# Performance work log

Hardware: AMD Instinct MI355X
Metric: run time of the kernel (lower is better)

Reference implementation:

```python
import jax, jax.numpy as jnp
import numpy as np

N = 100000   # nodes
E = 1000000  # edges
F_IN = 128
H = 64
L = 6
C = 10
G = 64       # graphs in batch


def setup_inputs() -> dict:
    key = jax.random.key(0)
    ks = jax.random.split(key, 12)
    x = jax.random.normal(ks[0], (N, F_IN), dtype=jnp.float32)
    edge_index = jax.random.randint(ks[1], (2, E), 0, N, dtype=jnp.int64)
    batch = jnp.sort(jax.random.randint(ks[2], (N,), 0, G, dtype=jnp.int64))
    s = lambda fan: 1.0 / np.sqrt(fan)
    return {
        "x": x,
        "edge_index": edge_index,
        "batch": batch,
        "W0": jax.random.normal(ks[3], (F_IN, H), dtype=jnp.float32) * s(F_IN),
        "b0": jnp.zeros((H,), jnp.float32),
        "Wh": jax.random.normal(ks[4], (L - 1, H, H), dtype=jnp.float32) * s(H),
        "bh": jnp.zeros((L - 1, H), jnp.float32),
        "jkW": jax.random.normal(ks[5], (H * L, H), dtype=jnp.float32) * s(H * L),
        "jkb": jnp.zeros((H,), jnp.float32),
        "W1": jax.random.normal(ks[6], (H, H), dtype=jnp.float32) * s(H),
        "b1": jnp.zeros((H,), jnp.float32),
        "W2": jax.random.normal(ks[7], (H, C), dtype=jnp.float32) * s(H),
        "b2": jnp.zeros((C,), jnp.float32),
    }


def reference(x, edge_index, batch, W0, b0, Wh, bh, jkW, jkb, W1, b1, W2, b2):
    n = x.shape[0]
    # add self-loops (PyG GCNConv default)
    loops = jnp.arange(n, dtype=edge_index.dtype)
    src = jnp.concatenate([edge_index[0], loops])
    dst = jnp.concatenate([edge_index[1], loops])
    # symmetric degree normalization D^{-1/2} (A+I) D^{-1/2}
    deg = jax.ops.segment_sum(jnp.ones_like(dst, x.dtype), dst, num_segments=n)
    disq = jnp.where(deg > 0, deg ** -0.5, 0.0)
    norm = (disq[src] * disq[dst])[:, None]  # [E+N, 1]

    def gcn(h, W, b):
        hW = h @ W                              # [N, H] transform first
        msg = hW[src] * norm                    # gather + normalize
        agg = jax.ops.segment_sum(msg, dst, num_segments=n)  # scatter-add
        return agg + b

    h = jax.nn.relu(gcn(x, W0, b0))
    xs = [h]
    for i in range(L - 1):
        h = jax.nn.relu(gcn(h, Wh[i], bh[i]))
        xs.append(h)
    hcat = jnp.concatenate(xs, axis=-1)         # JK 'cat' -> [N, H*L]
    h = jax.nn.relu(hcat @ jkW + jkb)
    pooled = jax.ops.segment_sum(h, batch, num_segments=G)  # global_add_pool
    h = jax.nn.relu(pooled @ W1 + b1)
    return jax.nn.softmax(h @ W2 + b2, axis=-1)  # [G, C]
```

## Files before the change

kernel.cpp:

```cpp
#include <hip/hip_runtime.h>
#include <hip/hip_fp16.h>

#define NN 100000
#define NE 1000000
#define F_INF 128
#define HID 64
#define NLAY 6
#define NCLS 10
#define NGRAPH 64
#define PART_SZ 12500

__device__ __forceinline__ float4 h4f(ushort4 u) {
    __half2 lo = *reinterpret_cast<__half2*>(&u);
    __half2 hi = *reinterpret_cast<__half2*>(reinterpret_cast<unsigned short*>(&u) + 2);
    float2 a = __half22float2(lo);
    float2 b = __half22float2(hi);
    return make_float4(a.x, a.y, b.x, b.y);
}

__device__ __forceinline__ ushort4 f4h(float4 v) {
    __half2 lo = __floats2half2_rn(v.x, v.y);
    __half2 hi = __floats2half2_rn(v.z, v.w);
    ushort4 u;
    *reinterpret_cast<__half2*>(&u) = lo;
    *reinterpret_cast<__half2*>(reinterpret_cast<unsigned short*>(&u) + 2) = hi;
    return u;
}

__global__ void k_hist(const int* __restrict__ dst, int* __restrict__ counts, int e) {
    int i = blockIdx.x * 256 + threadIdx.x;
    if (i < e) atomicAdd(&counts[dst[i]], 1);
}

__global__ void k_blocksum(const int* __restrict__ counts, int* __restrict__ bsum, int n) {
    int i = blockIdx.x * 256 + threadIdx.x;
    int v = (i < n) ? counts[i] : 0;
    #pragma unroll
    for (int off = 32; off >= 1; off >>= 1) v += __shfl_down(v, off);
    __shared__ int ws[4];
    if ((threadIdx.x & 63) == 0) ws[threadIdx.x >> 6] = v;
    __syncthreads();
    if (threadIdx.x == 0) bsum[blockIdx.x] = ws[0] + ws[1] + ws[2] + ws[3];
}

__global__ void k_scanbsum(int* __restrict__ bsum, int nb) {
    __shared__ int sh[512];
    int t = threadIdx.x;
    int v = (t < nb) ? bsum[t] : 0;
    sh[t] = v; __syncthreads();
    for (int off = 1; off < 512; off <<= 1) {
        int x = (t >= off) ? sh[t - off] : 0;
        __syncthreads();
        sh[t] += x; __syncthreads();
    }
    if (t < nb) bsum[t] = sh[t] - v;
}

__global__ void k_scanwrite(const int* __restrict__ counts, const int* __restrict__ bsumx,
                            int* __restrict__ rowptr, int* __restrict__ wptr,
                            float* __restrict__ disq, int n, int e) {
    __shared__ int sh[256];
    int t = threadIdx.x;
    int i = blockIdx.x * 256 + t;
    int v = (i < n) ? counts[i] : 0;
    sh[t] = v; __syncthreads();
    for (int off = 1; off < 256; off <<= 1) {
        int x = (t >= off) ? sh[t - off] : 0;
        __syncthreads();
        sh[t] += x; __syncthreads();
    }
    int excl = sh[t] - v + bsumx[blockIdx.x];
    if (i < n) {
        rowptr[i] = excl;
        wptr[i]   = excl;
        disq[i]   = rsqrtf((float)(v + 1));
    }
    if (i == 0) rowptr[n] = e;
}

__global__ void k_scatter_part(const int* __restrict__ src, const int* __restrict__ dst,
                               int* __restrict__ wptr, int* __restrict__ csr, int e) {
    int part = blockIdx.x & 7;
    int i = (blockIdx.x >> 3) * 256 + threadIdx.x;
    if (i < e) {
        int d = dst[i];
        if (d / PART_SZ == part) {
            int pos = atomicAdd(&wptr[d], 1);
            csr[pos] = src[i];
        }
    }
}

__global__ __launch_bounds__(256) void k_gemm_dual(
    const float* __restrict__ A, int lda, int K,
    const float* __restrict__ W,
    const float* __restrict__ jkw,
    const float* __restrict__ disq,
    unsigned short* __restrict__ C16,
    float* __restrict__ jkacc,
    int jk_mode, int n)
{
    __shared__ float Ws[64 * 64];
    __shared__ float Ws2[64 * 64];
    __shared__ float As[64 * 68];
    const int tid  = threadIdx.x;
    const int col4 = (tid & 15) * 4;
    const int rowq = tid >> 4;
    const int base = blockIdx.x * 64;

    {
        #pragma unroll
        for (int i = 0; i < 4; i++) {
            float4 v = *(const float4*)(W + (size_t)(i * 256 + tid) * 4);
            *(float4*)(Ws + (size_t)(i * 256 + tid) * 4) = v;
        }
        if (jk_mode) {
            #pragma unroll
            for (int i = 0; i < 4; i++) {
                float4 v = *(const float4*)(jkw + (size_t)(i * 256 + tid) * 4);
                *(float4*)(Ws2 + (size_t)(i * 256 + tid) * 4) = v;
            }
        }
        #pragma unroll
        for (int rr = 0; rr < 4; rr++) {
            int row = base + rowq + rr * 16;
            float4 v = make_float4(0.f, 0.f, 0.f, 0.f);
            if (row < n) v = *(const float4*)(A + (size_t)row * lda + col4);
            *(float4*)(As + (size_t)(rowq + rr * 16) * 68 + col4) = v;
        }
    }
    __syncthreads();

    float4 acc[4], acc2[4];
    #pragma unroll
    for (int r = 0; r < 4; r++) {
        acc[r]  = make_float4(0.f, 0.f, 0.f, 0.f);
        acc2[r] = make_float4(0.f, 0.f, 0.f, 0.f);
    }

    for (int k0 = 0; k0 < K; k0 += 64) {
        const bool more = (k0 + 64) < K;
        float4 wreg[4], areg[4];
        if (more) {
            #pragma unroll
            for (int i = 0; i < 4; i++)
                wreg[i] = *(const float4*)(W + (size_t)(k0 + 64) * 64 + (i * 256 + tid) * 4);
            #pragma unroll
            for (int rr = 0; rr < 4; rr++) {
                int row = base + rowq + rr * 16;
                areg[rr] = make_float4(0.f, 0.f, 0.f, 0.f);
                if (row < n) areg[rr] = *(const float4*)(A + (size_t)row * lda + k0 + 64 + col4);
            }
        }
        if (jk_mode && k0 == 0) {
            #pragma unroll 4
            for (int k = 0; k < 64; k++) {
                float4 w  = *(const float4*)(Ws  + k * 64 + col4);
                float4 w2 = *(const float4*)(Ws2 + k * 64 + col4);
                float a0 = As[(rowq * 4 + 0) * 68 + k];
                float a1 = As[(rowq * 4 + 1) * 68 + k];
                float a2 = As[(rowq * 4 + 2) * 68 + k];
                float a3 = As[(rowq * 4 + 3) * 68 + k];
                acc[0].x = fmaf(a0, w.x, acc[0].x); acc[0].y = fmaf(a0, w.y, acc[0].y);
                acc[0].z = fmaf(a0, w.z, acc[0].z); acc[0].w = fmaf(a0, w.w, acc[0].w);
                acc[1].x = fmaf(a1, w.x, acc[1].x); acc[1].y = fmaf(a1, w.y, acc[1].y);
                acc[1].z = fmaf(a1, w.z, acc[1].z); acc[1].w = fmaf(a1, w.w, acc[1].w);
                acc[2].x = fmaf(a2, w.x, acc[2].x); acc[2].y = fmaf(a2, w.y, acc[2].y);
                acc[2].z = fmaf(a2, w.z, acc[2].z); acc[2].w = fmaf(a2, w.w, acc[2].w);
                acc[3].x = fmaf(a3, w.x, acc[3].x); acc[3].y = fmaf(a3, w.y, acc[3].y);
                acc[3].z = fmaf(a3, w.z, acc[3].z); acc[3].w = fmaf(a3, w.w, acc[3].w);
                acc2[0].x = fmaf(a0, w2.x, acc2[0].x); acc2[0].y = fmaf(a0, w2.y, acc2[0].y);
                acc2[0].z = fmaf(a0, w2.z, acc2[0].z); acc2[0].w = fmaf(a0, w2.w, acc2[0].w);
                acc2[1].x = fmaf(a1, w2.x, acc2[1].x); acc2[1].y = fmaf(a1, w2.y, acc2[1].y);
                acc2[1].z = fmaf(a1, w2.z, acc2[1].z); acc2[1].w = fmaf(a1, w2.w, acc2[1].w);
                acc2[2].x = fmaf(a2, w2.x, acc2[2].x); acc2[2].y = fmaf(a2, w2.y, acc2[2].y);
                acc2[2].z = fmaf(a2, w2.z, acc2[2].z); acc2[2].w = fmaf(a2, w2.w, acc2[2].w);
                acc2[3].x = fmaf(a3, w2.x, acc2[3].x); acc2[3].y = fmaf(a3, w2.y, acc2[3].y);
                acc2[3].z = fmaf(a3, w2.z, acc2[3].z); acc2[3].w = fmaf(a3, w2.w, acc2[3].w);
            }
        } else {
            #pragma unroll 8
            for (int k = 0; k < 64; k++) {
                float4 w = *(const float4*)(Ws + k * 64 + col4);
                float a0 = As[(rowq * 4 + 0) * 68 + k];
                float a1 = As[(rowq * 4 + 1) * 68 + k];
                float a2 = As[(rowq * 4 + 2) * 68 + k];
                float a3 = As[(rowq * 4 + 3) * 68 + k];
                acc[0].x = fmaf(a0, w.x, acc[0].x); acc[0].y = fmaf(a0, w.y, acc[0].y);
                acc[0].z = fmaf(a0, w.z, acc[0].z); acc[0].w = fmaf(a0, w.w, acc[0].w);
                acc[1].x = fmaf(a1, w.x, acc[1].x); acc[1].y = fmaf(a1, w.y, acc[1].y);
                acc[1].z = fmaf(a1, w.z, acc[1].z); acc[1].w = fmaf(a1, w.w, acc[1].w);
                acc[2].x = fmaf(a2, w.x, acc[2].x); acc[2].y = fmaf(a2, w.y, acc[2].y);
                acc[2].z = fmaf(a2, w.z, acc[2].z); acc[2].w = fmaf(a2, w.w, acc[2].w);
                acc[3].x = fmaf(a3, w.x, acc[3].x); acc[3].y = fmaf(a3, w.y, acc[3].y);
                acc[3].z = fmaf(a3, w.z, acc[3].z); acc[3].w = fmaf(a3, w.w, acc[3].w);
            }
        }
        __syncthreads();
        if (more) {
            #pragma unroll
            for (int i = 0; i < 4; i++)
                *(float4*)(Ws + (size_t)(i * 256 + tid) * 4) = wreg[i];
            #pragma unroll
            for (int rr = 0; rr < 4; rr++)
                *(float4*)(As + (size_t)(rowq + rr * 16) * 68 + col4) = areg[rr];
            __syncthreads();
        }
    }

    #pragma unroll
    for (int r = 0; r < 4; r++) {
        int row = base + rowq * 4 + r;
        if (row < n) {
            float s = disq[row];
            float4 o;
            o.x = acc[r].x * s; o.y = acc[r].y * s;
            o.z = acc[r].z * s; o.w = acc[r].w * s;
            ((ushort4*)C16)[(size_t)row * 16 + (tid & 15)] = f4h(o);
            if (jk_mode == 1) {
                *(float4*)(jkacc + (size_t)row * 64 + col4) = acc2[r];
            } else if (jk_mode == 2) {
                float4 p = *(const float4*)(jkacc + (size_t)row * 64 + col4);
                p.x += acc2[r].x; p.y += acc2[r].y;
                p.z += acc2[r].z; p.w += acc2[r].w;
                *(float4*)(jkacc + (size_t)row * 64 + col4) = p;
            }
        }
    }
}

__global__ __launch_bounds__(256) void k_gather(
    const int* __restrict__ rowptr, const int* __restrict__ csr,
    const unsigned short* __restrict__ hW16, const float* __restrict__ disq,
    const float* __restrict__ bias, float* __restrict__ hout, int n)
{
    const ushort4* hW4 = (const ushort4*)hW16;
    int wid  = (blockIdx.x * 256 + threadIdx.x) >> 6;
    if (wid >= n) return;
    int lane = threadIdx.x & 63;
    int fb = lane & 15;
    int es = lane >> 4;
    int j  = rowptr[wid];
    int r1 = rowptr[wid + 1];
    float4 v  = make_float4(0.f, 0.f, 0.f, 0.f);
    float4 v2 = make_float4(0.f, 0.f, 0.f, 0.f);
    if (es == 0) v = h4f(hW4[(size_t)wid * 16 + fb]);
    while (j < r1) {
        int cnt = min(r1 - j, 64);
        int idx = (lane < cnt) ? csr[j + lane] : 0;
        int jj = 0;
        for (; jj + 8 <= cnt; jj += 8) {
            int s0 = __shfl(idx, jj + es);
            int s1 = __shfl(idx, jj + 4 + es);
            float4 t0 = h4f(hW4[(size_t)s0 * 16 + fb]);
            float4 t1 = h4f(hW4[(size_t)s1 * 16 + fb]);
            v.x  += t0.x; v.y  += t0.y; v.z  += t0.z; v.w  += t0.w;
            v2.x += t1.x; v2.y += t1.y; v2.z += t1.z; v2.w += t1.w;
        }
        for (; jj < cnt; jj += 4) {
            int sidx = jj + es;
            int s = __shfl(idx, (sidx < cnt) ? sidx : 0);
            if (sidx < cnt) {
                float4 t = h4f(hW4[(size_t)s * 16 + fb]);
                v.x += t.x; v.y += t.y; v.z += t.z; v.w += t.w;
            }
        }
        j += cnt;
    }
    v.x += v2.x; v.y += v2.y; v.z += v2.z; v.w += v2.w;
    v.x += __shfl_xor(v.x, 16); v.y += __shfl_xor(v.y, 16);
    v.z += __shfl_xor(v.z, 16); v.w += __shfl_xor(v.w, 16);
    v.x += __shfl_xor(v.x, 32); v.y += __shfl_xor(v.y, 32);
    v.z += __shfl_xor(v.z, 32); v.w += __shfl_xor(v.w, 32);
    if (es == 0) {
        float s = disq[wid];
        float4 b = ((const float4*)bias)[fb];
        float4 o;
        o.x = fmaxf(fmaf(s, v.x, b.x), 0.f);
        o.y = fmaxf(fmaf(s, v.y, b.y), 0.f);
        o.z = fmaxf(fmaf(s, v.z, b.z), 0.f);
        o.w = fmaxf(fmaf(s, v.w, b.w), 0.f);
        ((float4*)hout)[(size_t)wid * 16 + fb] = o;
    }
}

__global__ __launch_bounds__(256) void k_jkfin_pool(
    const float* __restrict__ A,
    const float* __restrict__ W,
    const float* __restrict__ jkacc,
    const float* __restrict__ bias,
    const int* __restrict__ batch,
    float* __restrict__ pooled,
    int n)
{
    __shared__ float Ws[64 * 64];
    __shared__ float As[64 * 68];
    const int tid  = threadIdx.x;
    const int col4 = (tid & 15) * 4;
    const int rowq = tid >> 4;
    const int base = blockIdx.x * 64;

    #pragma unroll
    for (int i = 0; i < 4; i++) {
        float4 v = *(const float4*)(W + (size_t)(i * 256 + tid) * 4);
        *(float4*)(Ws + (size_t)(i * 256 + tid) * 4) = v;
    }
    #pragma unroll
    for (int rr = 0; rr < 4; rr++) {
        int row = base + rowq + rr * 16;
        float4 v = make_float4(0.f, 0.f, 0.f, 0.f);
        if (row < n) v = *(const float4*)(A + (size_t)row * 64 + col4);
        *(float4*)(As + (size_t)(rowq + rr * 16) * 68 + col4) = v;
    }
    __syncthreads();

    float4 acc[4];
    #pragma unroll
    for (int r = 0; r < 4; r++) acc[r] = make_float4(0.f, 0.f, 0.f, 0.f);
    #pragma unroll 8
    for (int k = 0; k < 64; k++) {
        float4 w = *(const float4*)(Ws + k * 64 + col4);
        float a0 = As[(rowq * 4 + 0) * 68 + k];
        float a1 = As[(rowq * 4 + 1) * 68 + k];
        float a2 = As[(rowq * 4 + 2) * 68 + k];
        float a3 = As[(rowq * 4 + 3) * 68 + k];
        acc[0].x = fmaf(a0, w.x, acc[0].x); acc[0].y = fmaf(a0, w.y, acc[0].y);
        acc[0].z = fmaf(a0, w.z, acc[0].z); acc[0].w = fmaf(a0, w.w, acc[0].w);
        acc[1].x = fmaf(a1, w.x, acc[1].x); acc[1].y = fmaf(a1, w.y, acc[1].y);
        acc[1].z = fmaf(a1, w.z, acc[1].z); acc[1].w = fmaf(a1, w.w, acc[1].w);
        acc[2].x = fmaf(a2, w.x, acc[2].x); acc[2].y = fmaf(a2, w.y, acc[2].y);
        acc[2].z = fmaf(a2, w.z, acc[2].z); acc[2].w = fmaf(a2, w.w, acc[2].w);
        acc[3].x = fmaf(a3, w.x, acc[3].x); acc[3].y = fmaf(a3, w.y, acc[3].y);
        acc[3].z = fmaf(a3, w.z, acc[3].z); acc[3].w = fmaf(a3, w.w, acc[3].w);
    }
    __syncthreads();

    float* slab = Ws;
    #pragma unroll
    for (int i = tid; i < 4096; i += 256) slab[i] = 0.f;
    __syncthreads();

    float4 bb = *(const float4*)(bias + col4);
    int curg = -1;
    float4 s4 = make_float4(0.f, 0.f, 0.f, 0.f);
    #pragma unroll
    for (int r = 0; r < 4; r++) {
        int row = base + rowq * 4 + r;
        if (row < n) {
            float4 p = *(const float4*)(jkacc + (size_t)row * 64 + col4);
            float4 vv;
            vv.x = fmaxf(acc[r].x + p.x + bb.x, 0.f);
            vv.y = fmaxf(acc[r].y + p.y + bb.y, 0.f);
            vv.z = fmaxf(acc[r].z + p.z + bb.z, 0.f);
            vv.w = fmaxf(acc[r].w + p.w + bb.w, 0.f);
            int g = batch[row];
            if (g != curg) {
                if (curg >= 0) {
                    atomicAdd(&slab[curg * 64 + col4 + 0], s4.x);
                    atomicAdd(&slab[curg * 64 + col4 + 1], s4.y);
                    atomicAdd(&slab[curg * 64 + col4 + 2], s4.z);
                    atomicAdd(&slab[curg * 64 + col4 + 3], s4.w);
                }
                curg = g; s4 = vv;
            } else {
                s4.x += vv.x; s4.y += vv.y; s4.z += vv.z; s4.w += vv.w;
            }
        }
    }
    if (curg >= 0) {
        atomicAdd(&slab[curg * 64 + col4 + 0], s4.x);
        atomicAdd(&slab[curg * 64 + col4 + 1], s4.y);
        atomicAdd(&slab[curg * 64 + col4 + 2], s4.z);
        atomicAdd(&slab[curg * 64 + col4 + 3], s4.w);
    }
    __syncthreads();

    int g0 = batch[base];
    int g1 = batch[(base + 63 < n) ? (base + 63) : (n - 1)];
    int cnt = (g1 - g0 + 1) * 64;
    for (int i = tid; i < cnt; i += 256) {
        int g = g0 + (i >> 6);
        int c = i & 63;
        float v = slab[g * 64 + c];
        if (v != 0.f) atomicAdd(&pooled[g * 64 + c], v);
    }
}

__global__ __launch_bounds__(64) void k_head(
    const float* __restrict__ pooled,
    const float* __restrict__ W1, const float* __restrict__ b1,
    const float* __restrict__ W2, const float* __restrict__ b2,
    float* __restrict__ out)
{
    __shared__ float p[64];
    __shared__ float h1[64];
    __shared__ float lg[16];
    const int g = blockIdx.x;
    const int t = threadIdx.x;

    p[t] = pooled[g * 64 + t];
    __syncthreads();

    float acc = b1[t];
    #pragma unroll 8
    for (int k = 0; k < 64; k++) acc = fmaf(p[k], W1[k * 64 + t], acc);
    h1[t] = fmaxf(acc, 0.f);
    __syncthreads();

    if (t < NCLS) {
        float a = b2[t];
        #pragma unroll 8
        for (int j = 0; j < 64; j++) a = fmaf(h1[j], W2[j * NCLS + t], a);
        lg[t] = a;
    }
    __syncthreads();

    if (t == 0) {
        float mx = lg[0];
        #pragma unroll
        for (int c = 1; c < NCLS; c++) mx = fmaxf(mx, lg[c]);
        float ssum = 0.f;
        float e[NCLS];
        #pragma unroll
        for (int c = 0; c < NCLS; c++) { e[c] = __expf(lg[c] - mx); ssum += e[c]; }
        float inv = 1.0f / ssum;
        #pragma unroll
        for (int c = 0; c < NCLS; c++) out[g * NCLS + c] = e[c] * inv;
    }
}

extern "C" void kernel_launch(void* const* d_in, const int* in_sizes, int n_in,
                              void* d_out, int out_size, void* d_ws, size_t ws_size,
                              hipStream_t stream) {
    (void)in_sizes; (void)n_in; (void)out_size; (void)ws_size;
    const float* x     = (const float*)d_in[0];
    const int*   ei    = (const int*)d_in[1];
    const int*   batch = (const int*)d_in[2];
    const float* W0    = (const float*)d_in[3];
    const float* b0    = (const float*)d_in[4];
    const float* Wh    = (const float*)d_in[5];
    const float* bh    = (const float*)d_in[6];
    const float* jkW   = (const float*)d_in[7];
    const float* jkb   = (const float*)d_in[8];
    const float* W1    = (const float*)d_in[9];
    const float* b1    = (const float*)d_in[10];
    const float* W2    = (const float*)d_in[11];
    const float* b2    = (const float*)d_in[12];

    const int* src = ei;
    const int* dst = ei + NE;

    float*          fws   = (float*)d_ws;
    float*          disq  = fws;
    unsigned short* hWb   = (unsigned short*)(disq + 100352);
    float*          h     = (float*)(hWb + (size_t)NN * 64);
    float*          jkacc = h + (size_t)NN * 64;
    float*          pooled= jkacc + (size_t)NN * 64;
    int*            counts= (int*)(pooled + 4096);
    int*            rowptr= counts + 100352;
    int*            wptr  = rowptr + 100352;
    int*            bsum  = wptr + 100352;
    int*            csr   = bsum + 512;

    const int NB_N = (NN + 255) / 256;
    const int NB_E = (NE + 255) / 256;

    hipMemsetAsync(counts, 0, (size_t)NN * sizeof(int), stream);
    k_hist<<<NB_E, 256, 0, stream>>>(dst, counts, NE);
    k_blocksum<<<NB_N, 256, 0, stream>>>(counts, bsum, NN);
    k_scanbsum<<<1, 512, 0, stream>>>(bsum, NB_N);
    k_scanwrite<<<NB_N, 256, 0, stream>>>(counts, bsum, rowptr, wptr, disq, NN, NE);
    k_scatter_part<<<NB_E * 8, 256, 0, stream>>>(src, dst, wptr, csr, NE);

    const int gemm_grid   = (NN + 63) / 64;
    const int gather_grid = (NN + 3) / 4;
    for (int l = 0; l < NLAY; l++) {
        const float* A    = (l == 0) ? x : h;
        int          lda  = (l == 0) ? F_INF : HID;
        int          K    = (l == 0) ? F_INF : HID;
        const float* W    = (l == 0) ? W0 : (Wh + (size_t)(l - 1) * 64 * 64);
        const float* bias = (l == 0) ? b0 : (bh + (size_t)(l - 1) * 64);
        const float* jw   = (l == 0) ? nullptr : (jkW + (size_t)(l - 1) * 64 * 64);
        int          jkm  = (l == 0) ? 0 : ((l == 1) ? 1 : 2);

        k_gemm_dual<<<gemm_grid, 256, 0, stream>>>(A, lda, K, W, jw, disq,
                                                   hWb, jkacc, jkm, NN);
        k_gather<<<gather_grid, 256, 0, stream>>>(rowptr, csr, hWb, disq, bias, h, NN);
    }

    hipMemsetAsync(pooled, 0, 64 * 64 * sizeof(float), stream);
    k_jkfin_pool<<<gemm_grid, 256, 0, stream>>>(h, jkW + (size_t)5 * 64 * 64, jkacc,
                                                jkb, batch, pooled, NN);
    k_head<<<NGRAPH, 64, 0, stream>>>(pooled, W1, b1, W2, b2, (float*)d_out);
}
```

Before: 558.1 us.

## Store layer activations in fp16 and unroll gather loop to four edges

Layer outputs h are now written by the gather kernel as fp16 and read back as fp16 by the next layer's GEMM and by the final JK/pool kernel. This halves the activation write and read traffic per layer. The gather inner loop is also restructured to issue four neighbor loads per iteration with predicated accumulation, replacing the 8-step loop plus tail. In exchange, activations lose precision and the tail iterations waste some loads on masked lanes.

```diff
diff --git a/kernel.cpp b/kernel.cpp
--- a/kernel.cpp
+++ b/kernel.cpp
@@ -92,13 +92,13 @@
 }
 
 __global__ __launch_bounds__(256) void k_gemm_dual(
-    const float* __restrict__ A, int lda, int K,
+    const void* __restrict__ Araw, int lda, int K,
     const float* __restrict__ W,
     const float* __restrict__ jkw,
     const float* __restrict__ disq,
     unsigned short* __restrict__ C16,
     float* __restrict__ jkacc,
-    int jk_mode, int n)
+    int jk_mode, int a16, int n)
 {
     __shared__ float Ws[64 * 64];
     __shared__ float Ws2[64 * 64];
@@ -121,12 +121,24 @@
                 *(float4*)(Ws2 + (size_t)(i * 256 + tid) * 4) = v;
             }
         }
-        #pragma unroll
-        for (int rr = 0; rr < 4; rr++) {
-            int row = base + rowq + rr * 16;
-            float4 v = make_float4(0.f, 0.f, 0.f, 0.f);
-            if (row < n) v = *(const float4*)(A + (size_t)row * lda + col4);
-            *(float4*)(As + (size_t)(rowq + rr * 16) * 68 + col4) = v;
+        if (a16) {
+            const ushort4* Ah = (const ushort4*)Araw;
+            #pragma unroll
+            for (int rr = 0; rr < 4; rr++) {
+                int row = base + rowq + rr * 16;
+                float4 v = make_float4(0.f, 0.f, 0.f, 0.f);
+                if (row < n) v = h4f(Ah[(size_t)row * 16 + (tid & 15)]);
+                *(float4*)(As + (size_t)(rowq + rr * 16) * 68 + col4) = v;
+            }
+        } else {
+            const float* Af = (const float*)Araw;
+            #pragma unroll
+            for (int rr = 0; rr < 4; rr++) {
+                int row = base + rowq + rr * 16;
+                float4 v = make_float4(0.f, 0.f, 0.f, 0.f);
+                if (row < n) v = *(const float4*)(Af + (size_t)row * lda + col4);
+                *(float4*)(As + (size_t)(rowq + rr * 16) * 68 + col4) = v;
+            }
         }
     }
     __syncthreads();
@@ -142,6 +154,7 @@
         const bool more = (k0 + 64) < K;
         float4 wreg[4], areg[4];
         if (more) {
+            const float* Af = (const float*)Araw;
             #pragma unroll
             for (int i = 0; i < 4; i++)
                 wreg[i] = *(const float4*)(W + (size_t)(k0 + 64) * 64 + (i * 256 + tid) * 4);
@@ -149,7 +162,7 @@
             for (int rr = 0; rr < 4; rr++) {
                 int row = base + rowq + rr * 16;
                 areg[rr] = make_float4(0.f, 0.f, 0.f, 0.f);
-                if (row < n) areg[rr] = *(const float4*)(A + (size_t)row * lda + k0 + 64 + col4);
+                if (row < n) areg[rr] = *(const float4*)(Af + (size_t)row * lda + k0 + 64 + col4);
             }
         }
         if (jk_mode && k0 == 0) {
@@ -232,7 +245,7 @@
 __global__ __launch_bounds__(256) void k_gather(
     const int* __restrict__ rowptr, const int* __restrict__ csr,
     const unsigned short* __restrict__ hW16, const float* __restrict__ disq,
-    const float* __restrict__ bias, float* __restrict__ hout, int n)
+    const float* __restrict__ bias, unsigned short* __restrict__ hout16, int n)
 {
     const ushort4* hW4 = (const ushort4*)hW16;
     int wid  = (blockIdx.x * 256 + threadIdx.x) >> 6;
@@ -248,22 +261,20 @@
     while (j < r1) {
         int cnt = min(r1 - j, 64);
         int idx = (lane < cnt) ? csr[j + lane] : 0;
-        int jj = 0;
-        for (; jj + 8 <= cnt; jj += 8) {
-            int s0 = __shfl(idx, jj + es);
-            int s1 = __shfl(idx, jj + 4 + es);
+        for (int jj = 0; jj < cnt; jj += 16) {
+            int i0 = jj + es, i1 = jj + 4 + es, i2 = jj + 8 + es, i3 = jj + 12 + es;
+            int s0 = __shfl(idx, i0 & 63);
+            int s1 = __shfl(idx, i1 & 63);
+            int s2 = __shfl(idx, i2 & 63);
+            int s3 = __shfl(idx, i3 & 63);
             float4 t0 = h4f(hW4[(size_t)s0 * 16 + fb]);
             float4 t1 = h4f(hW4[(size_t)s1 * 16 + fb]);
-            v.x  += t0.x; v.y  += t0.y; v.z  += t0.z; v.w  += t0.w;
-            v2.x += t1.x; v2.y += t1.y; v2.z += t1.z; v2.w += t1.w;
-        }
-        for (; jj < cnt; jj += 4) {
-            int sidx = jj + es;
-            int s = __shfl(idx, (sidx < cnt) ? sidx : 0);
-            if (sidx < cnt) {
-                float4 t = h4f(hW4[(size_t)s * 16 + fb]);
-                v.x += t.x; v.y += t.y; v.z += t.z; v.w += t.w;
-            }
+            float4 t2 = h4f(hW4[(size_t)s2 * 16 + fb]);
+            float4 t3 = h4f(hW4[(size_t)s3 * 16 + fb]);
+            if (i0 < cnt) { v.x  += t0.x; v.y  += t0.y; v.z  += t0.z; v.w  += t0.w; }
+            if (i1 < cnt) { v2.x += t1.x; v2.y += t1.y; v2.z += t1.z; v2.w += t1.w; }
+            if (i2 < cnt) { v.x  += t2.x; v.y  += t2.y; v.z  += t2.z; v.w  += t2.w; }
+            if (i3 < cnt) { v2.x += t3.x; v2.y += t3.y; v2.z += t3.z; v2.w += t3.w; }
         }
         j += cnt;
     }
@@ -280,12 +291,12 @@
         o.y = fmaxf(fmaf(s, v.y, b.y), 0.f);
         o.z = fmaxf(fmaf(s, v.z, b.z), 0.f);
         o.w = fmaxf(fmaf(s, v.w, b.w), 0.f);
-        ((float4*)hout)[(size_t)wid * 16 + fb] = o;
+        ((ushort4*)hout16)[(size_t)wid * 16 + fb] = f4h(o);
     }
 }
 
 __global__ __launch_bounds__(256) void k_jkfin_pool(
-    const float* __restrict__ A,
+    const unsigned short* __restrict__ A16,
     const float* __restrict__ W,
     const float* __restrict__ jkacc,
     const float* __restrict__ bias,
@@ -305,12 +316,15 @@
         float4 v = *(const float4*)(W + (size_t)(i * 256 + tid) * 4);
         *(float4*)(Ws + (size_t)(i * 256 + tid) * 4) = v;
     }
-    #pragma unroll
-    for (int rr = 0; rr < 4; rr++) {
-        int row = base + rowq + rr * 16;
-        float4 v = make_float4(0.f, 0.f, 0.f, 0.f);
-        if (row < n) v = *(const float4*)(A + (size_t)row * 64 + col4);
-        *(float4*)(As + (size_t)(rowq + rr * 16) * 68 + col4) = v;
+    {
+        const ushort4* Ah = (const ushort4*)A16;
+        #pragma unroll
+        for (int rr = 0; rr < 4; rr++) {
+            int row = base + rowq + rr * 16;
+            float4 v = make_float4(0.f, 0.f, 0.f, 0.f);
+            if (row < n) v = h4f(Ah[(size_t)row * 16 + (tid & 15)]);
+            *(float4*)(As + (size_t)(rowq + rr * 16) * 68 + col4) = v;
+        }
     }
     __syncthreads();
 
@@ -450,17 +464,17 @@
     const int* src = ei;
     const int* dst = ei + NE;
 
-    float*          fws   = (float*)d_ws;
-    float*          disq  = fws;
-    unsigned short* hWb   = (unsigned short*)(disq + 100352);
-    float*          h     = (float*)(hWb + (size_t)NN * 64);
-    float*          jkacc = h + (size_t)NN * 64;
-    float*          pooled= jkacc + (size_t)NN * 64;
-    int*            counts= (int*)(pooled + 4096);
-    int*            rowptr= counts + 100352;
-    int*            wptr  = rowptr + 100352;
-    int*            bsum  = wptr + 100352;
-    int*            csr   = bsum + 512;
+    float*          fws    = (float*)d_ws;
+    float*          disq   = fws;
+    unsigned short* hWb    = (unsigned short*)(disq + 100352);
+    unsigned short* h16    = hWb + (size_t)NN * 64;
+    float*          jkacc  = (float*)(h16 + (size_t)NN * 64);
+    float*          pooled = jkacc + (size_t)NN * 64;
+    int*            counts = (int*)(pooled + 4096);
+    int*            rowptr = counts + 100352;
+    int*            wptr   = rowptr + 100352;
+    int*            bsum   = wptr + 100352;
+    int*            csr    = bsum + 512;
 
     const int NB_N = (NN + 255) / 256;
     const int NB_E = (NE + 255) / 256;
@@ -475,7 +489,8 @@
     const int gemm_grid   = (NN + 63) / 64;
     const int gather_grid = (NN + 3) / 4;
     for (int l = 0; l < NLAY; l++) {
-        const float* A    = (l == 0) ? x : h;
+        const void*  A    = (l == 0) ? (const void*)x : (const void*)h16;
+        int          a16  = (l == 0) ? 0 : 1;
         int          lda  = (l == 0) ? F_INF : HID;
         int          K    = (l == 0) ? F_INF : HID;
         const float* W    = (l == 0) ? W0 : (Wh + (size_t)(l - 1) * 64 * 64);
@@ -484,12 +499,12 @@
         int          jkm  = (l == 0) ? 0 : ((l == 1) ? 1 : 2);
 
         k_gemm_dual<<<gemm_grid, 256, 0, stream>>>(A, lda, K, W, jw, disq,
-                                                   hWb, jkacc, jkm, NN);
-        k_gather<<<gather_grid, 256, 0, stream>>>(rowptr, csr, hWb, disq, bias, h, NN);
+                                                   hWb, jkacc, jkm, a16, NN);
+        k_gather<<<gather_grid, 256, 0, stream>>>(rowptr, csr, hWb, disq, bias, h16, NN);
     }
 
     hipMemsetAsync(pooled, 0, 64 * 64 * sizeof(float), stream);
-    k_jkfin_pool<<<gemm_grid, 256, 0, stream>>>(h, jkW + (size_t)5 * 64 * 64, jkacc,
+    k_jkfin_pool<<<gemm_grid, 256, 0, stream>>>(h16, jkW + (size_t)5 * 64 * 64, jkacc,
                                                 jkb, batch, pooled, NN);
     k_head<<<NGRAPH, 64, 0, stream>>>(pooled, W1, b1, W2, b2, (float*)d_out);
 }
```

After: 550.7 us. About the same (-1.3%).
